# Kernel optimization log

Hardware: AMD Instinct MI355X
Metric: run time of the kernel (lower is better)

Reference implementation:

```python
import jax, jax.numpy as jnp
import numpy as np

N_NODES = 4_194_304
N_GRAPHS = 65_536

# Orthonormal (Frobenius) basis for symmetric traceless 3x3 matrices: the
# real l=2 components of 1o x 1o -> 2e (Clebsch-Gordan up to basis choice).
_s2 = 1.0 / np.sqrt(2.0)
_B = np.zeros((5, 3, 3), dtype=np.float32)
_B[0, 0, 1] = _B[0, 1, 0] = _s2            # xy
_B[1, 1, 2] = _B[1, 2, 1] = _s2            # yz
_B[2, 0, 2] = _B[2, 2, 0] = _s2            # xz
_B[3, 0, 0] = _s2; _B[3, 1, 1] = -_s2      # x^2 - y^2
_B[4, 0, 0] = _B[4, 1, 1] = -1.0 / np.sqrt(6.0); _B[4, 2, 2] = 2.0 / np.sqrt(6.0)
B_CG = jnp.asarray(_B)

INV_SQRT2 = 0.7071067811865476
INV_SQRT3 = 0.5773502691896258


def setup_inputs() -> dict:
    key = jax.random.key(0)
    k1, k2, k3, k4, k5, k6 = jax.random.split(key, 6)
    z = jax.random.randint(k1, (N_NODES,), 0, 100, dtype=jnp.int32)
    pos = jax.random.normal(k2, (N_NODES, 3), dtype=jnp.float32)
    batch = jnp.sort(jax.random.randint(k3, (N_NODES,), 0, N_GRAPHS, dtype=jnp.int32))
    # FullyConnectedTensorProduct weights: 5 paths, mul pattern (1,1,mul_out)
    # 0e*0e->2x0e (2) + 1o*1o->2x0e (2) + 0e*1o->2x1o (2) + 1o*0e->2x1o (2) + 1o*1o->1x2e (1) = 9
    w_tp = jax.random.normal(k4, (9,), dtype=jnp.float32)
    fc_w = jax.random.normal(k5, (1, 13), dtype=jnp.float32) / np.sqrt(13.0)
    fc_b = jax.random.normal(k6, (1,), dtype=jnp.float32) * 0.01
    return {"z": z, "pos": pos, "batch": batch, "w_tp": w_tp, "fc_w": fc_w, "fc_b": fc_b}


def reference(z, pos, batch, w_tp, fc_w, fc_b):
    s = z.astype(jnp.float32)                      # [N] scalar (0e) part
    v = pos                                        # [N,3] vector (1o) part
    wA, wB = w_tp[0:2], w_tp[2:4]                  # -> 2x0e paths
    wC, wD = w_tp[4:6], w_tp[6:8]                  # -> 2x1o paths
    wE = w_tp[8]                                   # -> 1x2e path

    # CG tensor product x (x) x -> 2x0e + 2x1o + 1x2e, path-normalized by 1/sqrt(#paths)
    ss = s * s                                     # 0e x 0e -> 0e
    dot = jnp.sum(v * v, axis=-1)                  # 1o . 1o -> 0e (CG = delta/sqrt3)
    out0 = (ss[:, None] * wA + (dot * INV_SQRT3)[:, None] * wB) * INV_SQRT2   # [N,2]
    sv = s[:, None] * v                            # 0e x 1o -> 1o
    out1 = (sv[:, None, :] * (wC + wD)[None, :, None]) * INV_SQRT2            # [N,2,3]
    quad = jnp.einsum('kij,ni,nj->nk', B_CG, v, v) # 1o x 1o -> 2e            # [N,5]
    out2 = wE * quad

    x = jnp.concatenate([out0, out1.reshape(-1, 6), out2], axis=-1)  # [N,13]
    x = jax.nn.relu(x)                             # (as in source: relu on all irreps)
    y = x @ fc_w.T + fc_b                          # [N,1] -> 1x0e
    y = jnp.tanh(y)                                # Gate on pure scalars = scalar act

    sums = jax.ops.segment_sum(y, batch, num_segments=N_GRAPHS)                # [G,1]
    counts = jax.ops.segment_sum(jnp.ones((batch.shape[0], 1), y.dtype), batch,
                                 num_segments=N_GRAPHS)
    return sums / jnp.maximum(counts, 1.0)
```

## Files before the change

kernel.cpp:

```cpp
#include <hip/hip_runtime.h>

static constexpr float INV_SQRT2 = 0.70710678118654752f;
static constexpr float INV_SQRT3 = 0.57735026918962576f;
static constexpr float SQRT2     = 1.41421356237309505f;
static constexpr float INV_SQRT6 = 0.40824829046386302f;

static constexpr int W_GRAPHS = 8;

__global__ __launch_bounds__(256) void e3nn_fused(
    const int*   __restrict__ z,
    const float* __restrict__ pos,
    const int*   __restrict__ batch,
    const float* __restrict__ w_tp,
    const float* __restrict__ fc_w,
    const float* __restrict__ fc_b,
    float*       __restrict__ out,
    int n, int n_graphs)
{
    const int lane = threadIdx.x & 63;
    const int wave = (blockIdx.x * blockDim.x + threadIdx.x) >> 6;
    const int g0   = wave * W_GRAPHS;
    if (g0 >= n_graphs) return;

    const float wA0 = w_tp[0], wA1 = w_tp[1];
    const float wB0 = w_tp[2], wB1 = w_tp[3];
    const float c0  = (w_tp[4] + w_tp[6]) * INV_SQRT2;
    const float c1  = (w_tp[5] + w_tp[7]) * INV_SQRT2;
    const float wE  = w_tp[8];
    float fw[13];
#pragma unroll
    for (int j = 0; j < 13; ++j) fw[j] = fc_w[j];
    const float fb = fc_b[0];

    const int tl     = (lane < W_GRAPHS) ? lane : W_GRAPHS;
    const int target = g0 + tl;
    unsigned p2 = 1;
    while (p2 < (unsigned)n) p2 <<= 1;
    int bval = 0;
    for (unsigned step = p2 >> 1; step > 0; step >>= 1) {
        const unsigned cand = (unsigned)bval + step;
        if (cand <= (unsigned)n && batch[cand - 1] < target) bval = (int)cand;
    }

    const int nb = __shfl_down(bval, 1);
    const int B0 = __shfl(bval, 0), B1 = __shfl(bval, 1);
    const int B2 = __shfl(bval, 2), B3 = __shfl(bval, 3);
    const int B4 = __shfl(bval, 4), B5 = __shfl(bval, 5);
    const int B6 = __shfl(bval, 6), B7 = __shfl(bval, 7);
    const int B8 = __shfl(bval, 8);

    float a0 = 0.f, a1 = 0.f, a2 = 0.f, a3 = 0.f;
    float a4 = 0.f, a5 = 0.f, a6 = 0.f, a7 = 0.f;

#pragma unroll 1
    for (int base = B0; base < B8; base += 64) {
        const int i = base + lane;
        if (i < B8) {
            const float sc = (float)z[i];
            const float v0 = pos[i * 3 + 0];
            const float v1 = pos[i * 3 + 1];
            const float v2 = pos[i * 3 + 2];

            const float ss   = sc * sc;
            const float dot3 = (v0 * v0 + v1 * v1 + v2 * v2) * INV_SQRT3;

            const float x0 = (ss * wA0 + dot3 * wB0) * INV_SQRT2;
            const float x1 = (ss * wA1 + dot3 * wB1) * INV_SQRT2;

            const float sv0 = sc * v0, sv1 = sc * v1, sv2 = sc * v2;
            const float x2 = sv0 * c0, x3 = sv1 * c0, x4 = sv2 * c0;
            const float x5 = sv0 * c1, x6 = sv1 * c1, x7 = sv2 * c1;

            const float x8  = wE * (SQRT2 * v0 * v1);
            const float x9  = wE * (SQRT2 * v1 * v2);
            const float x10 = wE * (SQRT2 * v0 * v2);
            const float x11 = wE * (INV_SQRT2 * (v0 * v0 - v1 * v1));
            const float x12 = wE * (INV_SQRT6 * (2.f * v2 * v2 - v0 * v0 - v1 * v1));

            float acc = fb;
            acc += fmaxf(x0,  0.f) * fw[0];
            acc += fmaxf(x1,  0.f) * fw[1];
            acc += fmaxf(x2,  0.f) * fw[2];
            acc += fmaxf(x3,  0.f) * fw[3];
            acc += fmaxf(x4,  0.f) * fw[4];
            acc += fmaxf(x5,  0.f) * fw[5];
            acc += fmaxf(x6,  0.f) * fw[6];
            acc += fmaxf(x7,  0.f) * fw[7];
            acc += fmaxf(x8,  0.f) * fw[8];
            acc += fmaxf(x9,  0.f) * fw[9];
            acc += fmaxf(x10, 0.f) * fw[10];
            acc += fmaxf(x11, 0.f) * fw[11];
            acc += fmaxf(x12, 0.f) * fw[12];
            const float y = tanhf(acc);

            const int gi = (i >= B1) + (i >= B2) + (i >= B3) + (i >= B4)
                         + (i >= B5) + (i >= B6) + (i >= B7);
            a0 += (gi == 0) ? y : 0.f;
            a1 += (gi == 1) ? y : 0.f;
            a2 += (gi == 2) ? y : 0.f;
            a3 += (gi == 3) ? y : 0.f;
            a4 += (gi == 4) ? y : 0.f;
            a5 += (gi == 5) ? y : 0.f;
            a6 += (gi == 6) ? y : 0.f;
            a7 += (gi == 7) ? y : 0.f;
        }
    }

#pragma unroll
    for (int off = 32; off >= 1; off >>= 1) {
        a0 += __shfl_xor(a0, off);
        a1 += __shfl_xor(a1, off);
        a2 += __shfl_xor(a2, off);
        a3 += __shfl_xor(a3, off);
        a4 += __shfl_xor(a4, off);
        a5 += __shfl_xor(a5, off);
        a6 += __shfl_xor(a6, off);
        a7 += __shfl_xor(a7, off);
    }

    if (lane < W_GRAPHS && g0 + lane < n_graphs) {
        float sel = (lane == 0) ? a0
                  : (lane == 1) ? a1
                  : (lane == 2) ? a2
                  : (lane == 3) ? a3
                  : (lane == 4) ? a4
                  : (lane == 5) ? a5
                  : (lane == 6) ? a6
                  :               a7;
        const float c = (float)(nb - bval);
        out[g0 + lane] = sel / fmaxf(c, 1.0f);
    }
}

extern "C" void kernel_launch(void* const* d_in, const int* in_sizes, int n_in,
                              void* d_out, int out_size, void* d_ws, size_t ws_size,
                              hipStream_t stream) {
    const int*   z     = (const int*)d_in[0];
    const float* pos   = (const float*)d_in[1];
    const int*   batch = (const int*)d_in[2];
    const float* w_tp  = (const float*)d_in[3];
    const float* fc_w  = (const float*)d_in[4];
    const float* fc_b  = (const float*)d_in[5];

    float* out = (float*)d_out;
    const int n        = in_sizes[0];
    const int n_graphs = out_size;

    const int waves = (n_graphs + W_GRAPHS - 1) / W_GRAPHS;
    const int blocks = (waves * 64 + 255) / 256;
    e3nn_fused<<<blocks, 256, 0, stream>>>(z, pos, batch, w_tp, fc_w, fc_b,
                                           out, n, n_graphs);
}
```

Before: 31.80 us.

## Fold weights into sign-gated coefficients and use fast exp-based tanh

Precomputes per-sign combined coefficients so that relu(a*x)*w becomes a select plus one FMA per feature, merging the two vector paths into a single term per component. Replaces tanhf with an exp2/rcp approximation and computes segment membership with boolean masks instead of an index sum. This cuts ALU work per node, at some risk to accuracy at large inputs from the approximate tanh.

New measurement: 27.61 us. 1.15x faster.

```diff
diff --git a/kernel.cpp b/kernel.cpp
--- a/kernel.cpp
+++ b/kernel.cpp
@@ -6,6 +6,15 @@
 static constexpr float INV_SQRT6 = 0.40824829046386302f;
 
 static constexpr int W_GRAPHS = 8;
+
+__device__ __forceinline__ float fast_tanh(float x) {
+    const float e = __builtin_amdgcn_exp2f(x * 2.8853900817779268f);
+    const float r = __builtin_amdgcn_rcpf(e + 1.0f);
+    return fmaf(-2.0f, r, 1.0f);
+}
+
+__device__ __forceinline__ float gate_p(float k, float fw) { return k > 0.f ? k * fw : 0.f; }
+__device__ __forceinline__ float gate_n(float k, float fw) { return k < 0.f ? k * fw : 0.f; }
 
 __global__ __launch_bounds__(256) void e3nn_fused(
     const int*   __restrict__ z,
@@ -22,15 +31,28 @@
     const int g0   = wave * W_GRAPHS;
     if (g0 >= n_graphs) return;
 
-    const float wA0 = w_tp[0], wA1 = w_tp[1];
-    const float wB0 = w_tp[2], wB1 = w_tp[3];
+    const float kA0 = w_tp[0] * INV_SQRT2;
+    const float kA1 = w_tp[1] * INV_SQRT2;
+    const float kB0 = w_tp[2] * (INV_SQRT3 * INV_SQRT2);
+    const float kB1 = w_tp[3] * (INV_SQRT3 * INV_SQRT2);
     const float c0  = (w_tp[4] + w_tp[6]) * INV_SQRT2;
     const float c1  = (w_tp[5] + w_tp[7]) * INV_SQRT2;
     const float wE  = w_tp[8];
-    float fw[13];
-#pragma unroll
-    for (int j = 0; j < 13; ++j) fw[j] = fc_w[j];
-    const float fb = fc_b[0];
+    const float fw0 = fc_w[0], fw1 = fc_w[1];
+    const float fb  = fc_b[0];
+
+    const float P0 = gate_p(c0, fc_w[2]) + gate_p(c1, fc_w[5]);
+    const float N0 = gate_n(c0, fc_w[2]) + gate_n(c1, fc_w[5]);
+    const float P1 = gate_p(c0, fc_w[3]) + gate_p(c1, fc_w[6]);
+    const float N1 = gate_n(c0, fc_w[3]) + gate_n(c1, fc_w[6]);
+    const float P2 = gate_p(c0, fc_w[4]) + gate_p(c1, fc_w[7]);
+    const float N2 = gate_n(c0, fc_w[4]) + gate_n(c1, fc_w[7]);
+    const float k8  = wE * SQRT2,     k11 = wE * INV_SQRT2, k12 = wE * INV_SQRT6;
+    const float P8  = gate_p(k8,  fc_w[8]),  N8  = gate_n(k8,  fc_w[8]);
+    const float P9  = gate_p(k8,  fc_w[9]),  N9  = gate_n(k8,  fc_w[9]);
+    const float P10 = gate_p(k8,  fc_w[10]), N10 = gate_n(k8,  fc_w[10]);
+    const float P11 = gate_p(k11, fc_w[11]), N11 = gate_n(k11, fc_w[11]);
+    const float P12 = gate_p(k12, fc_w[12]), N12 = gate_n(k12, fc_w[12]);
 
     const int tl     = (lane < W_GRAPHS) ? lane : W_GRAPHS;
     const int target = g0 + tl;
@@ -61,48 +83,44 @@
             const float v1 = pos[i * 3 + 1];
             const float v2 = pos[i * 3 + 2];
 
-            const float ss   = sc * sc;
-            const float dot3 = (v0 * v0 + v1 * v1 + v2 * v2) * INV_SQRT3;
+            const float v00 = v0 * v0, v11 = v1 * v1, v22 = v2 * v2;
+            const float ss  = sc * sc;
+            const float dr  = v00 + v11 + v22;
 
-            const float x0 = (ss * wA0 + dot3 * wB0) * INV_SQRT2;
-            const float x1 = (ss * wA1 + dot3 * wB1) * INV_SQRT2;
+            float acc = fb;
+            const float x0 = fmaf(ss, kA0, dr * kB0);
+            const float x1 = fmaf(ss, kA1, dr * kB1);
+            acc = fmaf(fmaxf(x0, 0.f), fw0, acc);
+            acc = fmaf(fmaxf(x1, 0.f), fw1, acc);
 
             const float sv0 = sc * v0, sv1 = sc * v1, sv2 = sc * v2;
-            const float x2 = sv0 * c0, x3 = sv1 * c0, x4 = sv2 * c0;
-            const float x5 = sv0 * c1, x6 = sv1 * c1, x7 = sv2 * c1;
+            acc = fmaf(sv0, (sv0 > 0.f ? P0 : N0), acc);
+            acc = fmaf(sv1, (sv1 > 0.f ? P1 : N1), acc);
+            acc = fmaf(sv2, (sv2 > 0.f ? P2 : N2), acc);
 
-            const float x8  = wE * (SQRT2 * v0 * v1);
-            const float x9  = wE * (SQRT2 * v1 * v2);
-            const float x10 = wE * (SQRT2 * v0 * v2);
-            const float x11 = wE * (INV_SQRT2 * (v0 * v0 - v1 * v1));
-            const float x12 = wE * (INV_SQRT6 * (2.f * v2 * v2 - v0 * v0 - v1 * v1));
+            const float t8 = v0 * v1, t9 = v1 * v2, t10 = v0 * v2;
+            acc = fmaf(t8,  (t8  > 0.f ? P8  : N8 ), acc);
+            acc = fmaf(t9,  (t9  > 0.f ? P9  : N9 ), acc);
+            acc = fmaf(t10, (t10 > 0.f ? P10 : N10), acc);
 
-            float acc = fb;
-            acc += fmaxf(x0,  0.f) * fw[0];
-            acc += fmaxf(x1,  0.f) * fw[1];
-            acc += fmaxf(x2,  0.f) * fw[2];
-            acc += fmaxf(x3,  0.f) * fw[3];
-            acc += fmaxf(x4,  0.f) * fw[4];
-            acc += fmaxf(x5,  0.f) * fw[5];
-            acc += fmaxf(x6,  0.f) * fw[6];
-            acc += fmaxf(x7,  0.f) * fw[7];
-            acc += fmaxf(x8,  0.f) * fw[8];
-            acc += fmaxf(x9,  0.f) * fw[9];
-            acc += fmaxf(x10, 0.f) * fw[10];
-            acc += fmaxf(x11, 0.f) * fw[11];
-            acc += fmaxf(x12, 0.f) * fw[12];
-            const float y = tanhf(acc);
+            const float t11 = v00 - v11;
+            acc = fmaf(t11, (t11 > 0.f ? P11 : N11), acc);
+            const float t12 = (v22 - v00) + (v22 - v11);
+            acc = fmaf(t12, (t12 > 0.f ? P12 : N12), acc);
 
-            const int gi = (i >= B1) + (i >= B2) + (i >= B3) + (i >= B4)
-                         + (i >= B5) + (i >= B6) + (i >= B7);
-            a0 += (gi == 0) ? y : 0.f;
-            a1 += (gi == 1) ? y : 0.f;
-            a2 += (gi == 2) ? y : 0.f;
-            a3 += (gi == 3) ? y : 0.f;
-            a4 += (gi == 4) ? y : 0.f;
-            a5 += (gi == 5) ? y : 0.f;
-            a6 += (gi == 6) ? y : 0.f;
-            a7 += (gi == 7) ? y : 0.f;
+            const float y = fast_tanh(acc);
+
+            const bool ge1 = i >= B1, ge2 = i >= B2, ge3 = i >= B3;
+            const bool ge4 = i >= B4, ge5 = i >= B5, ge6 = i >= B6;
+            const bool ge7 = i >= B7;
+            a0 += (!ge1)        ? y : 0.f;
+            a1 += (ge1 && !ge2) ? y : 0.f;
+            a2 += (ge2 && !ge3) ? y : 0.f;
+            a3 += (ge3 && !ge4) ? y : 0.f;
+            a4 += (ge4 && !ge5) ? y : 0.f;
+            a5 += (ge5 && !ge6) ? y : 0.f;
+            a6 += (ge6 && !ge7) ? y : 0.f;
+            a7 += (ge7)         ? y : 0.f;
         }
     }
 
```
